# Optimization experiments

Measured on AMD Instinct MI355X. Metric: run time of the kernel, lower is better.

Reference implementation:

```python
import jax, jax.numpy as jnp
import numpy as np

B, A, NC, DIR, LMAX, MAXZ, NORB = 8, 64, 128, 4, 2, 10, 14
NF = NC * DIR * (2 * LMAX + 1)   # 2560
O2 = NORB * NORB                 # 196
AO = A * NORB                    # 896
LOG2 = float(np.log(2.0))

def ssp(v):  # spk shifted softplus
    return jax.nn.softplus(v) - LOG2

def setup_inputs():
    key = jax.random.key(0)
    ks = jax.random.split(key, 12)
    Z = jax.random.randint(ks[0], (B, A), 1, MAXZ)
    idx = np.arange(A)
    nbh_np = np.stack([np.delete(idx, i) for i in range(A)], 0)  # [A, A-1]: all atoms except self
    nbh = jnp.asarray(np.broadcast_to(nbh_np[None], (B, A, A - 1)).copy(), dtype=jnp.int32)
    x = jax.random.normal(ks[1], (B, A, NC), jnp.float32)
    Vijkl = jax.random.normal(ks[2], (B, A, A - 1, NF), jnp.float32) * 0.1
    sc = 1.0 / np.sqrt(NF)
    W_off = jax.random.normal(ks[3], (NF, O2), jnp.float32) * sc
    b_off = jnp.zeros((O2,), jnp.float32)
    W_on = jax.random.normal(ks[4], (NF, O2), jnp.float32) * sc
    b_on = jnp.zeros((O2,), jnp.float32)
    W_ovoff = jax.random.normal(ks[5], (NF, O2), jnp.float32) * sc
    b_ovoff = jnp.zeros((O2,), jnp.float32)
    ov_emb = jax.random.normal(ks[6], (MAXZ, O2), jnp.float32) * 0.1  # trainable overlap onsite embedding
    orb_energies = jax.random.normal(ks[7], (MAXZ, NORB), jnp.float32)  # h0 energies
    s0_energies = jnp.ones((MAXZ, NORB), jnp.float32)                   # s0 init = ones
    W1 = jax.random.normal(ks[8], (NC, NC // 2), jnp.float32) / np.sqrt(NC)
    b1 = jnp.zeros((NC // 2,), jnp.float32)
    W2 = jax.random.normal(ks[9], (NC // 2, 1), jnp.float32) / np.sqrt(NC // 2)
    b2 = jnp.zeros((1,), jnp.float32)
    return {"Z": Z, "nbh": nbh, "x": x, "Vijkl": Vijkl,
            "W_off": W_off, "b_off": b_off, "W_on": W_on, "b_on": b_on,
            "W_ovoff": W_ovoff, "b_ovoff": b_ovoff, "ov_emb": ov_emb,
            "orb_energies": orb_energies, "s0_energies": s0_energies,
            "W1": W1, "b1": b1, "W2": W2, "b2": b2}

def reference(Z, nbh, x, Vijkl, W_off, b_off, W_on, b_on, W_ovoff, b_ovoff,
              ov_emb, orb_energies, s0_energies, W1, b1, W2, b2):
    # permutation that reorders neighbor slots (plus appended zero/self slot) into atom order
    ar = jnp.broadcast_to(jnp.arange(A, dtype=nbh.dtype)[None, :, None], (B, A, 1))
    sort_idx = jnp.argsort(jnp.concatenate([nbh, ar], axis=2), axis=2)  # [B,A,A]
    eyeA = jnp.eye(A, dtype=Vijkl.dtype)
    eyeAO = jnp.eye(AO, dtype=Vijkl.dtype)

    def assemble(off, on):
        # off: [B,A,A-1,O2] pair blocks; on: [B,A,O2] onsite blocks
        offz = jnp.concatenate([off, jnp.zeros((B, A, 1, O2), off.dtype)], axis=2)  # zero self block at slot A-1
        offg = jnp.take_along_axis(offz, sort_idx[..., None], axis=2)               # [B,A,A,O2]
        M = offg + eyeA[None, :, :, None] * on[:, :, None, :]
        M = M.reshape(B, A, A, NORB, NORB).transpose(0, 1, 3, 2, 4).reshape(B, AO, AO)
        return 0.5 * (M + M.transpose(0, 2, 1))

    # Hamiltonian: offsite Dense + onsite Dense mean-aggregated over pairs
    H_off = Vijkl @ W_off + b_off                       # [B,A,A-1,O2]
    H_on = jnp.mean(Vijkl @ W_on + b_on, axis=2)        # [B,A,O2]
    H = assemble(H_off, H_on)
    # h0 single-atom diagonal (orb mask is all-active -> full diagonal)
    H = H + eyeAO[None] * orb_energies[Z].reshape(B, 1, AO)

    # Overlap: offsite Dense + onsite embedding lookup
    S_off = Vijkl @ W_ovoff + b_ovoff
    S_on = ov_emb[Z]                                    # [B,A,O2]
    S = assemble(S_off, S_on)
    S = S + eyeAO[None] * s0_energies[Z].reshape(B, 1, AO)

    # energy head: Dense->ssp->Dense->ScaleShift(0,1), sum over atoms
    Ei = ssp(x @ W1 + b1) @ W2 + b2                     # [B,A,1]
    E = jnp.sum(Ei, axis=1)                             # [B,1]
    return H, S, E
```

## Files before the change

kernel.cpp:

```cpp
#include <hip/hip_runtime.h>

#define B_      8
#define A_      64
#define NPAIR   63
#define NC_     128
#define NF_     2560
#define O2_     196
#define NORB_   14
#define AO_     896
#define NCOLS   588
#define CSTRIDE 640
#define KSTEPS  80
#define BM      128
#define BN      640
#define BSTEP_BYTES 40960

typedef short bf16x8 __attribute__((ext_vector_type(8)));
typedef float f32x4  __attribute__((ext_vector_type(4)));

__device__ __forceinline__ unsigned f2bf(float f) {
    unsigned u = __builtin_bit_cast(unsigned, f);
    return (u + 0x7fffu + ((u >> 16) & 1u)) >> 16;
}

__global__ __launch_bounds__(512)
void prep_energy(const float* __restrict__ W_off, const float* __restrict__ W_ovoff,
                 const float* __restrict__ W_on, unsigned short* __restrict__ Bws,
                 const float* __restrict__ x, const float* __restrict__ W1,
                 const float* __restrict__ b1, const float* __restrict__ W2,
                 const float* __restrict__ b2, float* __restrict__ E) {
    const int t = threadIdx.x;
    if (blockIdx.x < KSTEPS) {
        __shared__ float wt[32 * BN];
        const int ks = blockIdx.x;
        for (int e = t; e < 32 * BN; e += 512) {
            int kl = e / BN, c = e - kl * BN;
            int kg = ks * 32 + kl;
            float v = 0.f;
            if (c < O2_)          v = W_off  [(size_t)kg * O2_ + c];
            else if (c < 2 * O2_) v = W_ovoff[(size_t)kg * O2_ + (c - O2_)];
            else if (c < 3 * O2_) v = W_on   [(size_t)kg * O2_ + (c - 2 * O2_)];
            wt[kl * BN + c] = v;
        }
        __syncthreads();
        unsigned short* out = Bws + (size_t)ks * (BN * 32);
        for (int e = t; e < BN * 4; e += 512) {
            int n = e >> 2, sg = e & 3;
            uint4 w;
            w.x = f2bf(wt[(sg * 8 + 0) * BN + n]) | (f2bf(wt[(sg * 8 + 1) * BN + n]) << 16);
            w.y = f2bf(wt[(sg * 8 + 2) * BN + n]) | (f2bf(wt[(sg * 8 + 3) * BN + n]) << 16);
            w.z = f2bf(wt[(sg * 8 + 4) * BN + n]) | (f2bf(wt[(sg * 8 + 5) * BN + n]) << 16);
            w.w = f2bf(wt[(sg * 8 + 6) * BN + n]) | (f2bf(wt[(sg * 8 + 7) * BN + n]) << 16);
            *(uint4*)(out + (size_t)n * 32 + sg * 8) = w;
        }
    } else {
        __shared__ float partial[8];
        const int b = blockIdx.x - KSTEPS;
        const int lane = t & 63;
        const int w = t >> 6;
        float esum = 0.f;
        for (int aa = 0; aa < 8; ++aa) {
            const int a = w * 8 + aa;
            const float* xr = x + (size_t)(b * A_ + a) * NC_;
            float hj = b1[lane];
            for (int k = 0; k < NC_; ++k) hj = fmaf(xr[k], W1[k * 64 + lane], hj);
            float sp = fmaxf(hj, 0.f) + log1pf(expf(-fabsf(hj))) - 0.69314718055994531f;
            float v = sp * W2[lane];
            for (int off = 32; off; off >>= 1) v += __shfl_down(v, off);
            if (lane == 0) esum += v + b2[0];
        }
        if (lane == 0) partial[w] = esum;
        __syncthreads();
        if (t == 0) {
            float e = 0.f;
            for (int k = 0; k < 8; ++k) e += partial[k];
            E[b] = e;
        }
    }
}

__global__ __launch_bounds__(1024, 4)
void gemm_off(const float* __restrict__ V, const unsigned short* __restrict__ Bws,
              const float* __restrict__ b_off, const float* __restrict__ b_ovoff,
              const float* __restrict__ b_on, float* __restrict__ HSoff) {
    __shared__ alignas(16) float          Af32[2][BM * 32];
    __shared__ alignas(16) unsigned short Ab16[2][BM * 32];

    const int tid  = threadIdx.x;
    const int mt   = blockIdx.x;
    const int lane = tid & 63;
    const int wv   = tid >> 6;
    const int wm   = wv >> 3, wn = wv & 7;
    const int wvu  = __builtin_amdgcn_readfirstlane(wv);

    const float* asrc = V + (size_t)(mt * BM + (tid >> 3)) * NF_ + (tid & 7) * 4;

    const char* bp = (const char*)Bws + (size_t)(wn * 80 + (lane & 15)) * 64 + (lane >> 4) * 16;
#define BFRAG(t_, nf_) (*(const bf16x8*)(bp + (size_t)(t_) * BSTEP_BYTES + (nf_) * 1024))

    f32x4 acc[4][5];
#pragma unroll
    for (int mf = 0; mf < 4; ++mf)
#pragma unroll
        for (int nf = 0; nf < 5; ++nf)
            acc[mf][nf] = (f32x4){0.f, 0.f, 0.f, 0.f};

    auto stage = [&](int buf, int t) {
        __builtin_amdgcn_global_load_lds(
            (const __attribute__((address_space(1))) void*)(asrc + (size_t)t * 32),
            (__attribute__((address_space(3))) void*)(&Af32[buf][wvu * 256]), 16, 0, 0);
    };

    const int crr = tid >> 3, cq = tid & 7;
    const int csl = ((cq >> 1) + ((crr + (crr >> 2)) & 3)) & 3;
    const unsigned cdst = (unsigned)(crr * 64 + csl * 16 + (cq & 1) * 8);

    const unsigned klo4 = (unsigned)(lane >> 4);

#define AFRAG(abf_, mf_, Bb16_) {                                                   \
    const unsigned R_ = (unsigned)(wm * 64 + (lane & 15) + (mf_) * 16);             \
    const unsigned sl_ = (klo4 + ((R_ + (R_ >> 2)) & 3)) & 3;                       \
    abf_ = *(const bf16x8*)((const char*)(Bb16_) + R_ * 64 + sl_ * 16); }

#define MFMA1(abf_, bq_, mf_, nf_) \
    acc[mf_][nf_] = __builtin_amdgcn_mfma_f32_16x16x32_bf16(abf_, bq_, acc[mf_][nf_], 0, 0, 0);

    bf16x8 bq0, bq1, bq2, bq3, bq4, af0, af1, af2, af3;

    stage(0, 0);
    stage(1, 1);
    bq0 = BFRAG(0, 0); bq1 = BFRAG(0, 1); bq2 = BFRAG(0, 2); bq3 = BFRAG(0, 3); bq4 = BFRAG(0, 4);
    asm volatile("s_waitcnt vmcnt(6)" ::: "memory");
    {
        float4 cf = *(const float4*)((const char*)&Af32[0][0] + tid * 16);
        unsigned lo, hi;
        asm("v_cvt_pk_bf16_f32 %0, %1, %2" : "=v"(lo) : "v"(cf.x), "v"(cf.y));
        asm("v_cvt_pk_bf16_f32 %0, %1, %2" : "=v"(hi) : "v"(cf.z), "v"(cf.w));
        uint2 cw = {lo, hi};
        *(uint2*)((char*)&Ab16[0][0] + cdst) = cw;
    }
    asm volatile("s_waitcnt lgkmcnt(0)" ::: "memory");
    __builtin_amdgcn_s_barrier();
    __builtin_amdgcn_sched_barrier(0);

    for (int t = 0; t < KSTEPS; ++t) {
        const int buf = t & 1;
        if (t + 2 < KSTEPS) stage(buf, t + 2);

        AFRAG(af0, 0, &Ab16[buf][0]);
        AFRAG(af1, 1, &Ab16[buf][0]);
        __builtin_amdgcn_s_setprio(1);
        MFMA1(af0, bq0, 0, 0); MFMA1(af0, bq1, 0, 1); MFMA1(af0, bq2, 0, 2);
        MFMA1(af0, bq3, 0, 3); MFMA1(af0, bq4, 0, 4);
        MFMA1(af1, bq0, 1, 0); MFMA1(af1, bq1, 1, 1); MFMA1(af1, bq2, 1, 2);
        MFMA1(af1, bq3, 1, 3); MFMA1(af1, bq4, 1, 4);
        __builtin_amdgcn_s_setprio(0);

        if (t + 1 < KSTEPS) {
            asm volatile("s_waitcnt vmcnt(5)" ::: "memory");
            float4 cf = *(const float4*)((const char*)&Af32[buf ^ 1][0] + tid * 16);
            unsigned lo, hi;
            asm("v_cvt_pk_bf16_f32 %0, %1, %2" : "=v"(lo) : "v"(cf.x), "v"(cf.y));
            asm("v_cvt_pk_bf16_f32 %0, %1, %2" : "=v"(hi) : "v"(cf.z), "v"(cf.w));
            uint2 cw = {lo, hi};
            *(uint2*)((char*)&Ab16[buf ^ 1][0] + cdst) = cw;
        }

        AFRAG(af2, 2, &Ab16[buf][0]);
        AFRAG(af3, 3, &Ab16[buf][0]);
        __builtin_amdgcn_s_setprio(1);
        MFMA1(af2, bq0, 2, 0); MFMA1(af3, bq0, 3, 0); bq0 = BFRAG(t + 1, 0);
        MFMA1(af2, bq1, 2, 1); MFMA1(af3, bq1, 3, 1); bq1 = BFRAG(t + 1, 1);
        MFMA1(af2, bq2, 2, 2); MFMA1(af3, bq2, 3, 2); bq2 = BFRAG(t + 1, 2);
        MFMA1(af2, bq3, 2, 3); MFMA1(af3, bq3, 3, 3); bq3 = BFRAG(t + 1, 3);
        MFMA1(af2, bq4, 2, 4); MFMA1(af3, bq4, 3, 4); bq4 = BFRAG(t + 1, 4);
        __builtin_amdgcn_s_setprio(0);

        asm volatile("s_waitcnt lgkmcnt(0)" ::: "memory");
        __builtin_amdgcn_sched_barrier(0);
        __builtin_amdgcn_s_barrier();
        __builtin_amdgcn_sched_barrier(0);
    }

    const int c16 = lane & 15, rg = lane >> 4;
#pragma unroll
    for (int nf = 0; nf < 5; ++nf) {
        int C = wn * 80 + nf * 16 + c16;
        if (C >= NCOLS) continue;
        float bias = (C < O2_) ? b_off[C] : (C < 2 * O2_) ? b_ovoff[C - O2_] : b_on[C - 2 * O2_];
#pragma unroll
        for (int mf = 0; mf < 4; ++mf) {
            int R = mt * BM + wm * 64 + mf * 16 + rg * 4;
            float* o = HSoff + (size_t)R * CSTRIDE + C;
            o[0]           = acc[mf][nf][0] + bias;
            o[CSTRIDE]     = acc[mf][nf][1] + bias;
            o[2 * CSTRIDE] = acc[mf][nf][2] + bias;
            o[3 * CSTRIDE] = acc[mf][nf][3] + bias;
        }
    }
#undef BFRAG
#undef AFRAG
#undef MFMA1
}

__global__ void hon_reduce(const float* __restrict__ HSoff, float* __restrict__ Hon) {
    const int g = blockIdx.x;
    const int t = threadIdx.x;
    if (t >= O2_) return;
    const float* p0 = HSoff + (size_t)g * NPAIR * CSTRIDE + 2 * O2_ + t;
    const float* p1 = p0 + (size_t)21 * CSTRIDE;
    const float* p2 = p0 + (size_t)42 * CSTRIDE;
    float a0 = 0.f, a1 = 0.f, a2 = 0.f;
#pragma unroll 3
    for (int j = 0; j < 21; ++j) {
        a0 += p0[0]; a1 += p1[0]; a2 += p2[0];
        p0 += CSTRIDE; p1 += CSTRIDE; p2 += CSTRIDE;
    }
    Hon[(size_t)g * O2_ + t] = (a0 + a1 + a2) * (1.f / (float)NPAIR);
}

__global__ __launch_bounds__(256)
void assemble_k(const float* __restrict__ HSoff, const float* __restrict__ Hon,
                const int* __restrict__ Z, const float* __restrict__ ov_emb,
                const float* __restrict__ orbE, const float* __restrict__ s0E,
                float* __restrict__ H, float* __restrict__ S) {
    __shared__ float Ai[NPAIR * 197];
    __shared__ float Bj[2][16 * 200];
    __shared__ float Dg[O2_];
    __shared__ float Dd[NORB_];

    const int bid = blockIdx.x;
    const int h = bid & 1, i = (bid >> 1) & 63, b = bid >> 7;
    const int t = threadIdx.x;
    const int g = b * A_ + i;
    const int z = Z[g];
    float* out = (h ? S : H) + (size_t)b * AO_ * AO_;

    const float* abase = HSoff + (size_t)g * NPAIR * CSTRIDE + h * O2_;
    for (int u = t; u < NPAIR * O2_; u += 256) {
        int jj = u / O2_, e = u - jj * O2_;
        Ai[jj * 197 + e] = abase[(size_t)jj * CSTRIDE + e];
    }
    if (t < O2_)   Dg[t] = h ? ov_emb[(size_t)z * O2_ + t]   : Hon[(size_t)g * O2_ + t];
    if (t < NORB_) Dd[t] = h ? s0E[(size_t)z * NORB_ + t]    : orbE[(size_t)z * NORB_ + t];

    auto stageB = [&](int buf, int jc) {
        for (int u = t; u < 16 * O2_; u += 256) {
            int jl = u / O2_, e = u - jl * O2_;
            int j = jc * 16 + jl;
            if (j != i) {
                int idx = (i < j) ? i : i - 1;
                Bj[buf][jl * 200 + e] =
                    HSoff[((size_t)(b * A_ + j) * NPAIR + idx) * CSTRIDE + h * O2_ + e];
            }
        }
    };
    stageB(0, 0);
    __syncthreads();

    const int tj = t / NORB_, tq = t - tj * NORB_;
    for (int jc = 0; jc < 4; ++jc) {
        if (jc < 3) stageB((jc + 1) & 1, jc + 1);
        if (t < 224) {
            const int j = jc * 16 + tj;
            const int cur = jc & 1;
#pragma unroll
            for (int p = 0; p < NORB_; ++p) {
                float v;
                if (j == i) {
                    v = 0.5f * (Dg[p * NORB_ + tq] + Dg[tq * NORB_ + p]);
                    if (p == tq) v += Dd[p];
                } else {
                    int jj = (j < i) ? j : j - 1;
                    v = 0.5f * (Ai[jj * 197 + p * NORB_ + tq] + Bj[cur][tj * 200 + tq * NORB_ + p]);
                }
                out[(size_t)(i * NORB_ + p) * AO_ + jc * 224 + t] = v;
            }
        }
        __syncthreads();
    }
}

extern "C" void kernel_launch(void* const* d_in, const int* in_sizes, int n_in,
                              void* d_out, int out_size, void* d_ws, size_t ws_size,
                              hipStream_t stream) {
    const int*   Z       = (const int*)  d_in[0];
    const float* x       = (const float*)d_in[2];
    const float* V       = (const float*)d_in[3];
    const float* W_off   = (const float*)d_in[4];
    const float* b_off   = (const float*)d_in[5];
    const float* W_on    = (const float*)d_in[6];
    const float* b_on    = (const float*)d_in[7];
    const float* W_ovoff = (const float*)d_in[8];
    const float* b_ovoff = (const float*)d_in[9];
    const float* ov_emb  = (const float*)d_in[10];
    const float* orbE    = (const float*)d_in[11];
    const float* s0E     = (const float*)d_in[12];
    const float* W1      = (const float*)d_in[13];
    const float* b1      = (const float*)d_in[14];
    const float* W2      = (const float*)d_in[15];
    const float* b2      = (const float*)d_in[16];

    float* H = (float*)d_out;
    float* S = H + (size_t)B_ * AO_ * AO_;
    float* E = S + (size_t)B_ * AO_ * AO_;

    char* ws = (char*)d_ws;
    unsigned short* Bws = (unsigned short*)ws;
    float* HSoff = (float*)(ws + (size_t)4  * 1024 * 1024);
    float* Hon   = (float*)(ws + (size_t)88 * 1024 * 1024);

    prep_energy<<<KSTEPS + B_, 512, 0, stream>>>(W_off, W_ovoff, W_on, Bws,
                                                 x, W1, b1, W2, b2, E);
    gemm_off   <<<252,  1024, 0, stream>>>(V, Bws, b_off, b_ovoff, b_on, HSoff);
    hon_reduce <<<512,  256,  0, stream>>>(HSoff, Hon);
    assemble_k <<<1024, 256,  0, stream>>>(HSoff, Hon, Z, ov_emb, orbE, s0E, H, S);
}
```

Measured before the change: 269.4 us.

## Fuse onsite mean reduction into GEMM epilogue with atom-aligned 126-row tiles

The GEMM tile is resized to 126 rows (two atoms' worth of neighbor pairs) so each block can reduce the onsite-Hamiltonian columns in registers and LDS atomics and write Hon directly. This removes the separate hon_reduce kernel and the HSoff store and reload of 196 columns, and shrinks the HSoff stride from 640 to 400. The A-operand pipeline is deepened to four fp32 staging slots and three bf16 slots, converting two steps ahead. The cost is more LDS per block, idle threads in the last row group, and wasted MFMA rows (126 of 128 used).

```diff
diff --git a/kernel.cpp b/kernel.cpp
--- a/kernel.cpp
+++ b/kernel.cpp
@@ -9,9 +9,10 @@
 #define NORB_   14
 #define AO_     896
 #define NCOLS   588
-#define CSTRIDE 640
+#define NSTORE  392
+#define CSTRIDE 400
 #define KSTEPS  80
-#define BM      128
+#define BM      126
 #define BN      640
 #define BSTEP_BYTES 40960
 
@@ -82,9 +83,11 @@
 __global__ __launch_bounds__(1024, 4)
 void gemm_off(const float* __restrict__ V, const unsigned short* __restrict__ Bws,
               const float* __restrict__ b_off, const float* __restrict__ b_ovoff,
-              const float* __restrict__ b_on, float* __restrict__ HSoff) {
-    __shared__ alignas(16) float          Af32[2][BM * 32];
-    __shared__ alignas(16) unsigned short Ab16[2][BM * 32];
+              const float* __restrict__ b_on, float* __restrict__ HSoff,
+              float* __restrict__ Hon) {
+    __shared__ alignas(16) float          Af32[4][4096];
+    __shared__ alignas(16) unsigned short Ab16[3][4096];
+    __shared__ float HonLds[2][O2_];
 
     const int tid  = threadIdx.x;
     const int mt   = blockIdx.x;
@@ -92,6 +95,7 @@
     const int wv   = tid >> 6;
     const int wm   = wv >> 3, wn = wv & 7;
     const int wvu  = __builtin_amdgcn_readfirstlane(wv);
+    const bool sthr = tid < BM * 8;
 
     const float* asrc = V + (size_t)(mt * BM + (tid >> 3)) * NF_ + (tid & 7) * 4;
 
@@ -105,18 +109,28 @@
         for (int nf = 0; nf < 5; ++nf)
             acc[mf][nf] = (f32x4){0.f, 0.f, 0.f, 0.f};
 
-    auto stage = [&](int buf, int t) {
-        __builtin_amdgcn_global_load_lds(
-            (const __attribute__((address_space(1))) void*)(asrc + (size_t)t * 32),
-            (__attribute__((address_space(3))) void*)(&Af32[buf][wvu * 256]), 16, 0, 0);
+    auto stage = [&](int slot, int kk) {
+        if (sthr)
+            __builtin_amdgcn_global_load_lds(
+                (const __attribute__((address_space(1))) void*)(asrc + (size_t)kk * 32),
+                (__attribute__((address_space(3))) void*)(&Af32[slot][wvu * 256]), 16, 0, 0);
     };
 
     const int crr = tid >> 3, cq = tid & 7;
     const int csl = ((cq >> 1) + ((crr + (crr >> 2)) & 3)) & 3;
     const unsigned cdst = (unsigned)(crr * 64 + csl * 16 + (cq & 1) * 8);
+    auto conv = [&](int fslot, int bslot) {
+        if (sthr) {
+            float4 cf = *(const float4*)((const char*)&Af32[fslot][0] + tid * 16);
+            unsigned lo, hi;
+            asm("v_cvt_pk_bf16_f32 %0, %1, %2" : "=v"(lo) : "v"(cf.x), "v"(cf.y));
+            asm("v_cvt_pk_bf16_f32 %0, %1, %2" : "=v"(hi) : "v"(cf.z), "v"(cf.w));
+            uint2 cw = {lo, hi};
+            *(uint2*)((char*)&Ab16[bslot][0] + cdst) = cw;
+        }
+    };
 
     const unsigned klo4 = (unsigned)(lane >> 4);
-
 #define AFRAG(abf_, mf_, Bb16_) {                                                   \
     const unsigned R_ = (unsigned)(wm * 64 + (lane & 15) + (mf_) * 16);             \
     const unsigned sl_ = (klo4 + ((R_ + (R_ >> 2)) & 3)) & 3;                       \
@@ -125,98 +139,104 @@
 #define MFMA1(abf_, bq_, mf_, nf_) \
     acc[mf_][nf_] = __builtin_amdgcn_mfma_f32_16x16x32_bf16(abf_, bq_, acc[mf_][nf_], 0, 0, 0);
 
-    bf16x8 bq0, bq1, bq2, bq3, bq4, af0, af1, af2, af3;
-
-    stage(0, 0);
-    stage(1, 1);
+    bf16x8 bq0, bq1, bq2, bq3, bq4, abf;
+
+    stage(0, 0); stage(1, 1); stage(2, 2); stage(3, 3);
     bq0 = BFRAG(0, 0); bq1 = BFRAG(0, 1); bq2 = BFRAG(0, 2); bq3 = BFRAG(0, 3); bq4 = BFRAG(0, 4);
-    asm volatile("s_waitcnt vmcnt(6)" ::: "memory");
-    {
-        float4 cf = *(const float4*)((const char*)&Af32[0][0] + tid * 16);
-        unsigned lo, hi;
-        asm("v_cvt_pk_bf16_f32 %0, %1, %2" : "=v"(lo) : "v"(cf.x), "v"(cf.y));
-        asm("v_cvt_pk_bf16_f32 %0, %1, %2" : "=v"(hi) : "v"(cf.z), "v"(cf.w));
-        uint2 cw = {lo, hi};
-        *(uint2*)((char*)&Ab16[0][0] + cdst) = cw;
-    }
+    asm volatile("s_waitcnt vmcnt(8)" ::: "memory");
+    __builtin_amdgcn_sched_barrier(0);
+    conv(0, 0);
+    asm volatile("s_waitcnt vmcnt(7)" ::: "memory");
+    __builtin_amdgcn_sched_barrier(0);
+    conv(1, 1);
     asm volatile("s_waitcnt lgkmcnt(0)" ::: "memory");
     __builtin_amdgcn_s_barrier();
     __builtin_amdgcn_sched_barrier(0);
 
     for (int t = 0; t < KSTEPS; ++t) {
-        const int buf = t & 1;
-        if (t + 2 < KSTEPS) stage(buf, t + 2);
-
-        AFRAG(af0, 0, &Ab16[buf][0]);
-        AFRAG(af1, 1, &Ab16[buf][0]);
-        __builtin_amdgcn_s_setprio(1);
-        MFMA1(af0, bq0, 0, 0); MFMA1(af0, bq1, 0, 1); MFMA1(af0, bq2, 0, 2);
-        MFMA1(af0, bq3, 0, 3); MFMA1(af0, bq4, 0, 4);
-        MFMA1(af1, bq0, 1, 0); MFMA1(af1, bq1, 1, 1); MFMA1(af1, bq2, 1, 2);
-        MFMA1(af1, bq3, 1, 3); MFMA1(af1, bq4, 1, 4);
-        __builtin_amdgcn_s_setprio(0);
-
-        if (t + 1 < KSTEPS) {
-            asm volatile("s_waitcnt vmcnt(5)" ::: "memory");
-            float4 cf = *(const float4*)((const char*)&Af32[buf ^ 1][0] + tid * 16);
-            unsigned lo, hi;
-            asm("v_cvt_pk_bf16_f32 %0, %1, %2" : "=v"(lo) : "v"(cf.x), "v"(cf.y));
-            asm("v_cvt_pk_bf16_f32 %0, %1, %2" : "=v"(hi) : "v"(cf.z), "v"(cf.w));
-            uint2 cw = {lo, hi};
-            *(uint2*)((char*)&Ab16[buf ^ 1][0] + cdst) = cw;
-        }
-
-        AFRAG(af2, 2, &Ab16[buf][0]);
-        AFRAG(af3, 3, &Ab16[buf][0]);
-        __builtin_amdgcn_s_setprio(1);
-        MFMA1(af2, bq0, 2, 0); MFMA1(af3, bq0, 3, 0); bq0 = BFRAG(t + 1, 0);
-        MFMA1(af2, bq1, 2, 1); MFMA1(af3, bq1, 3, 1); bq1 = BFRAG(t + 1, 1);
-        MFMA1(af2, bq2, 2, 2); MFMA1(af3, bq2, 3, 2); bq2 = BFRAG(t + 1, 2);
-        MFMA1(af2, bq3, 2, 3); MFMA1(af3, bq3, 3, 3); bq3 = BFRAG(t + 1, 3);
-        MFMA1(af2, bq4, 2, 4); MFMA1(af3, bq4, 3, 4); bq4 = BFRAG(t + 1, 4);
-        __builtin_amdgcn_s_setprio(0);
-
+        if (t + 2 < KSTEPS) {
+            asm volatile("s_waitcnt vmcnt(6)" ::: "memory");
+            __builtin_amdgcn_sched_barrier(0);
+            conv((t + 2) & 3, (t + 2) % 3);
+        }
+
+        const unsigned short* At = &Ab16[t % 3][0];
+#pragma unroll
+        for (int mf = 0; mf < 4; ++mf) {
+            AFRAG(abf, mf, At);
+            __builtin_amdgcn_s_setprio(1);
+            MFMA1(abf, bq0, mf, 0); if (mf == 3) bq0 = BFRAG(t + 1, 0);
+            MFMA1(abf, bq1, mf, 1); if (mf == 3) bq1 = BFRAG(t + 1, 1);
+            MFMA1(abf, bq2, mf, 2); if (mf == 3) bq2 = BFRAG(t + 1, 2);
+            MFMA1(abf, bq3, mf, 3); if (mf == 3) bq3 = BFRAG(t + 1, 3);
+            MFMA1(abf, bq4, mf, 4); if (mf == 3) bq4 = BFRAG(t + 1, 4);
+            __builtin_amdgcn_s_setprio(0);
+        }
+
+        {
+            int kk = t + 4 < KSTEPS ? t + 4 : KSTEPS - 1;
+            stage((t + 4) & 3, kk);
+        }
         asm volatile("s_waitcnt lgkmcnt(0)" ::: "memory");
         __builtin_amdgcn_sched_barrier(0);
         __builtin_amdgcn_s_barrier();
         __builtin_amdgcn_sched_barrier(0);
     }
 
+    asm volatile("s_waitcnt vmcnt(0)" ::: "memory");
+    if (tid < 2 * O2_) HonLds[tid / O2_][tid % O2_] = 0.f;
+    __syncthreads();
+
     const int c16 = lane & 15, rg = lane >> 4;
 #pragma unroll
     for (int nf = 0; nf < 5; ++nf) {
-        int C = wn * 80 + nf * 16 + c16;
-        if (C >= NCOLS) continue;
-        float bias = (C < O2_) ? b_off[C] : (C < 2 * O2_) ? b_ovoff[C - O2_] : b_on[C - 2 * O2_];
+        const int C = wn * 80 + nf * 16 + c16;
+        if (C >= NSTORE) continue;
+        const float bias = (C < O2_) ? b_off[C] : b_ovoff[C - O2_];
 #pragma unroll
         for (int mf = 0; mf < 4; ++mf) {
-            int R = mt * BM + wm * 64 + mf * 16 + rg * 4;
-            float* o = HSoff + (size_t)R * CSTRIDE + C;
-            o[0]           = acc[mf][nf][0] + bias;
-            o[CSTRIDE]     = acc[mf][nf][1] + bias;
-            o[2 * CSTRIDE] = acc[mf][nf][2] + bias;
-            o[3 * CSTRIDE] = acc[mf][nf][3] + bias;
-        }
+            const int L = wm * 64 + mf * 16 + rg * 4;
+#pragma unroll
+            for (int jj = 0; jj < 4; ++jj) {
+                const int row = L + jj;
+                if (row < BM)
+                    HSoff[(size_t)(mt * BM + row) * CSTRIDE + C] = acc[mf][nf][jj] + bias;
+            }
+        }
+    }
+#pragma unroll
+    for (int nf = 0; nf < 5; ++nf) {
+        const int C = wn * 80 + nf * 16 + c16;
+        if (C < NSTORE || C >= NCOLS) continue;
+        const int cc = C - NSTORE;
+        float s0 = 0.f, s1 = 0.f;
+#pragma unroll
+        for (int mf = 0; mf < 4; ++mf) {
+            const int L = wm * 64 + mf * 16 + rg * 4;
+#pragma unroll
+            for (int jj = 0; jj < 4; ++jj) {
+                const int row = L + jj;
+                const float v = acc[mf][nf][jj];
+                if (row < NPAIR)            s0 += v;
+                else if (row < BM)          s1 += v;
+            }
+        }
+        s0 += __shfl_down(s0, 32); s0 += __shfl_down(s0, 16);
+        s1 += __shfl_down(s1, 32); s1 += __shfl_down(s1, 16);
+        if (lane < 16) {
+            atomicAdd(&HonLds[0][cc], s0);
+            atomicAdd(&HonLds[1][cc], s1);
+        }
+    }
+    __syncthreads();
+    if (tid < 2 * O2_) {
+        const int atom = tid / O2_, c = tid % O2_;
+        Hon[(size_t)(mt * 2 + atom) * O2_ + c] =
+            HonLds[atom][c] * (1.f / (float)NPAIR) + b_on[c];
     }
 #undef BFRAG
 #undef AFRAG
 #undef MFMA1
-}
-
-__global__ void hon_reduce(const float* __restrict__ HSoff, float* __restrict__ Hon) {
-    const int g = blockIdx.x;
-    const int t = threadIdx.x;
-    if (t >= O2_) return;
-    const float* p0 = HSoff + (size_t)g * NPAIR * CSTRIDE + 2 * O2_ + t;
-    const float* p1 = p0 + (size_t)21 * CSTRIDE;
-    const float* p2 = p0 + (size_t)42 * CSTRIDE;
-    float a0 = 0.f, a1 = 0.f, a2 = 0.f;
-#pragma unroll 3
-    for (int j = 0; j < 21; ++j) {
-        a0 += p0[0]; a1 += p1[0]; a2 += p2[0];
-        p0 += CSTRIDE; p1 += CSTRIDE; p2 += CSTRIDE;
-    }
-    Hon[(size_t)g * O2_ + t] = (a0 + a1 + a2) * (1.f / (float)NPAIR);
 }
 
 __global__ __launch_bounds__(256)
@@ -308,11 +328,10 @@
     char* ws = (char*)d_ws;
     unsigned short* Bws = (unsigned short*)ws;
     float* HSoff = (float*)(ws + (size_t)4  * 1024 * 1024);
-    float* Hon   = (float*)(ws + (size_t)88 * 1024 * 1024);
+    float* Hon   = (float*)(ws + (size_t)60 * 1024 * 1024);
 
     prep_energy<<<KSTEPS + B_, 512, 0, stream>>>(W_off, W_ovoff, W_on, Bws,
                                                  x, W1, b1, W2, b2, E);
-    gemm_off   <<<252,  1024, 0, stream>>>(V, Bws, b_off, b_ovoff, b_on, HSoff);
-    hon_reduce <<<512,  256,  0, stream>>>(HSoff, Hon);
+    gemm_off   <<<256,  1024, 0, stream>>>(V, Bws, b_off, b_ovoff, b_on, HSoff, Hon);
     assemble_k <<<1024, 256,  0, stream>>>(HSoff, Hon, Z, ov_emb, orbE, s0E, H, S);
 }
```

After: 252.6 us. 1.07x faster.
